# Performance work log

Measured on AMD Instinct MI355X. Metric: run time of the kernel, lower is better.

## Reference

```python
import jax, jax.numpy as jnp
import numpy as np

WINDOW = 512
STEP = 256
N_FREQ = 256
EPS = 1e-8


def setup_inputs() -> dict:
    key = jax.random.key(0)
    k1, k2, k3 = jax.random.split(key, 3)
    audio = jax.random.normal(k1, (512, 32768), dtype=jnp.float32)
    basis_real = jax.random.normal(k2, (N_FREQ, WINDOW), dtype=jnp.float32)
    basis_imag = jax.random.normal(k3, (N_FREQ, WINDOW), dtype=jnp.float32)
    return {"audio": audio, "basis_real": basis_real, "basis_imag": basis_imag}


def reference(audio, basis_real, basis_imag):
    # --- framing (windowed_audio): strided unfold -> [B, n_frames, WINDOW] ---
    n_samples = audio.shape[-1]
    n_frames = (n_samples - WINDOW) // STEP + 1  # 127 for 32768 samples
    idx = jnp.arange(n_frames)[:, None] * STEP + jnp.arange(WINDOW)[None, :]
    windowed = audio[:, idx]  # [B, F, W]

    # --- per-frame L2 normalization ---
    norms = jnp.linalg.norm(windowed, axis=-1, keepdims=True)  # [B, F, 1]
    wn = windowed / (norms + EPS)

    # --- basis normalization by complex L2 norm over window dim ---
    bnorm = jnp.sqrt(jnp.sum(basis_real * basis_real + basis_imag * basis_imag,
                             axis=-1, keepdims=True))  # [K, 1]
    br = basis_real / (bnorm + EPS)
    bi = basis_imag / (bnorm + EPS)

    # --- projection: windowed @ basis.T, real and imag parts ---
    real = jnp.einsum('bfw,kw->bfk', wn, br)  # [B, F, K]
    imag = jnp.einsum('bfw,kw->bfk', wn, bi)  # [B, F, K]
    return norms, real, imag
```

## Files before the change

### kernel.cpp

```cpp
#include <hip/hip_runtime.h>

#define WINDOW   512
#define STEPSZ   256
#define NFRAMES  127
#define NSAMP    32768
#define NBATCH   512
#define NFREQ    256
#define BM       64
#define SAMP_TILE 16640

typedef __attribute__((ext_vector_type(8))) short short8;
typedef __attribute__((ext_vector_type(4))) short bf16x4;
typedef __attribute__((ext_vector_type(4))) float f32x4;
typedef __attribute__((ext_vector_type(4))) float f4;

static __device__ __forceinline__ short f2bf(float x) {
    union { float f; unsigned u; } v; v.f = x;
    unsigned r = (v.u + 0x7fffu + ((v.u >> 16) & 1u)) >> 16;
    return (short)r;
}
static __device__ __forceinline__ float bf2f(short h) {
    union { unsigned u; float f; } v; v.u = ((unsigned)(unsigned short)h) << 16;
    return v.f;
}

__global__ __launch_bounds__(256) void prep_kernel(const float* __restrict__ br,
                                                   const float* __restrict__ bi,
                                                   short* __restrict__ Bf) {
    const int lane = threadIdx.x & 63;
    const int wid  = threadIdx.x >> 6;
    const int k    = blockIdx.x * 4 + wid;
    const float* pr = br + (size_t)k * WINDOW + lane * 8;
    const float* pi = bi + (size_t)k * WINDOW + lane * 8;
    f4 r0 = *(const f4*)pr;
    f4 r1 = *(const f4*)(pr + 4);
    f4 i0 = *(const f4*)pi;
    f4 i1 = *(const f4*)(pi + 4);
    float ss = 0.f;
#pragma unroll
    for (int j = 0; j < 4; ++j)
        ss += r0[j]*r0[j] + r1[j]*r1[j] + i0[j]*i0[j] + i1[j]*i1[j];
#pragma unroll
    for (int d = 1; d < 64; d <<= 1) ss += __shfl_xor(ss, d, 64);
    const float inv = 1.0f / (sqrtf(ss) + 1e-8f);
    short8 hr, hi;
#pragma unroll
    for (int j = 0; j < 4; ++j) {
        hr[j]     = f2bf(r0[j] * inv);
        hr[j + 4] = f2bf(r1[j] * inv);
        hi[j]     = f2bf(i0[j] * inv);
        hi[j + 4] = f2bf(i1[j] * inv);
    }
    const int kk = lane >> 2, kgrp = lane & 3;
    const int rl  = k & 15;
    const int ntR = k >> 4;
    const int ntI = 16 + (k >> 4);
    *(short8*)(Bf + ((size_t)(ntR * 16 + kk) * 64 + kgrp * 16 + rl) * 8) = hr;
    *(short8*)(Bf + ((size_t)(ntI * 16 + kk) * 64 + kgrp * 16 + rl) * 8) = hi;
}

__global__ __launch_bounds__(1024, 4) void mel_kernel(const float* __restrict__ audio,
                                                      const short* __restrict__ Bf,
                                                      float* __restrict__ out) {
    __shared__ short smp[SAMP_TILE];
    __shared__ float invn[BM];

    const int tid  = threadIdx.x;
    const int lane = tid & 63;
    const int wid  = tid >> 6;

    const int b   = blockIdx.x >> 1;
    const int mt0 = blockIdx.x & 1;
    const int f0  = mt0 * BM;

    float* out_norms = out;
    float* out_real  = out + 65024;
    float* out_imag  = out + 65024 + 16646144;

    const float* abase = audio + (size_t)b * NSAMP + f0 * STEPSZ;
    const int smax = NSAMP - f0 * STEPSZ - 4;

#pragma unroll
    for (int it = 0; it < 5; ++it) {
        const int sl = it * 4096 + tid * 4;
        if (sl < SAMP_TILE) {
            const int slc = sl < smax ? sl : smax;
            f4 v = *(const f4*)(abase + slc);
            bf16x4 h;
#pragma unroll
            for (int q = 0; q < 4; ++q) h[q] = f2bf(v[q]);
            const int byt = sl * 2;
            const int swz = byt ^ (((byt >> 9) & 7) << 4);
            *(bf16x4*)((char*)smp + swz) = h;
        }
    }
    __syncthreads();

    {
        const int f = tid >> 4, q = tid & 15;
        float ss = 0.f;
#pragma unroll
        for (int j = 0; j < 4; ++j) {
            const int byt = (f * 256 + q * 32 + j * 8) * 2;
            const int swz = byt ^ (((byt >> 9) & 7) << 4);
            short8 hv = *(const short8*)((const char*)smp + swz);
#pragma unroll
            for (int e = 0; e < 8; ++e) { const float x = bf2f(hv[e]); ss += x * x; }
        }
        ss += __shfl_xor(ss, 1, 64);
        ss += __shfl_xor(ss, 2, 64);
        ss += __shfl_xor(ss, 4, 64);
        ss += __shfl_xor(ss, 8, 64);
        const float nrm = sqrtf(ss);
        if (q == 0) {
            const int fr = f0 + f;
            if (fr < NFRAMES) out_norms[b * NFRAMES + fr] = nrm;
            invn[f] = 1.0f / (nrm + 1e-8f);
        }
    }
    __syncthreads();

    const int rlane = lane & 15;
    const int kgrp  = lane >> 4;
    const int ntg0  = wid * 2;

    f32x4 acc[4][2];
#pragma unroll
    for (int mt = 0; mt < 4; ++mt) { acc[mt][0] = (f32x4)0.f; acc[mt][1] = (f32x4)0.f; }

    const short* bp0 = Bf + ((size_t)(ntg0 + 0) * 16 * 64 + lane) * 8;
    const short* bp1 = Bf + ((size_t)(ntg0 + 1) * 16 * 64 + lane) * 8;
    short8 b0 = *(const short8*)bp0;
    short8 b1 = *(const short8*)bp1;

#pragma unroll 4
    for (int kk = 0; kk < 16; ++kk) {
        short8 a0, a1, a2, a3;
        {
            const int kb = kk * 64 + kgrp * 16;
            int byt;
            byt = (0 * 16 + rlane) * 512 + kb; a0 = *(const short8*)((const char*)smp + (byt ^ (((byt >> 9) & 7) << 4)));
            byt = (1 * 16 + rlane) * 512 + kb; a1 = *(const short8*)((const char*)smp + (byt ^ (((byt >> 9) & 7) << 4)));
            byt = (2 * 16 + rlane) * 512 + kb; a2 = *(const short8*)((const char*)smp + (byt ^ (((byt >> 9) & 7) << 4)));
            byt = (3 * 16 + rlane) * 512 + kb; a3 = *(const short8*)((const char*)smp + (byt ^ (((byt >> 9) & 7) << 4)));
        }
        short8 nb0 = b0, nb1 = b1;
        if (kk < 15) {
            nb0 = *(const short8*)(bp0 + (size_t)(kk + 1) * 512);
            nb1 = *(const short8*)(bp1 + (size_t)(kk + 1) * 512);
        }
        acc[0][0] = __builtin_amdgcn_mfma_f32_16x16x32_bf16(a0, b0, acc[0][0], 0, 0, 0);
        acc[1][0] = __builtin_amdgcn_mfma_f32_16x16x32_bf16(a1, b0, acc[1][0], 0, 0, 0);
        acc[2][0] = __builtin_amdgcn_mfma_f32_16x16x32_bf16(a2, b0, acc[2][0], 0, 0, 0);
        acc[3][0] = __builtin_amdgcn_mfma_f32_16x16x32_bf16(a3, b0, acc[3][0], 0, 0, 0);
        acc[0][1] = __builtin_amdgcn_mfma_f32_16x16x32_bf16(a0, b1, acc[0][1], 0, 0, 0);
        acc[1][1] = __builtin_amdgcn_mfma_f32_16x16x32_bf16(a1, b1, acc[1][1], 0, 0, 0);
        acc[2][1] = __builtin_amdgcn_mfma_f32_16x16x32_bf16(a2, b1, acc[2][1], 0, 0, 0);
        acc[3][1] = __builtin_amdgcn_mfma_f32_16x16x32_bf16(a3, b1, acc[3][1], 0, 0, 0);
        b0 = nb0; b1 = nb1;
    }

#pragma unroll
    for (int mt = 0; mt < 4; ++mt) {
        const int rbase = mt * 16 + kgrp * 4;
#pragma unroll
        for (int nt = 0; nt < 2; ++nt) {
            const int n = (ntg0 + nt) * 16 + rlane;
            float* dst = (n < NFREQ) ? out_real : out_imag;
            const int kcol = n & (NFREQ - 1);
#pragma unroll
            for (int j = 0; j < 4; ++j) {
                const int r  = rbase + j;
                const int fr = f0 + r;
                if (fr < NFRAMES)
                    dst[((size_t)b * NFRAMES + fr) * NFREQ + kcol] = acc[mt][nt][j] * invn[r];
            }
        }
    }
}

extern "C" void kernel_launch(void* const* d_in, const int* in_sizes, int n_in,
                              void* d_out, int out_size, void* d_ws, size_t ws_size,
                              hipStream_t stream) {
    const float* audio = (const float*)d_in[0];
    const float* br    = (const float*)d_in[1];
    const float* bi    = (const float*)d_in[2];
    float* out = (float*)d_out;
    short* Bf  = (short*)d_ws;

    prep_kernel<<<64, 256, 0, stream>>>(br, bi, Bf);
    mel_kernel<<<NBATCH * 2, 1024, 0, stream>>>(audio, Bf, out);
}
```

Measured before the change: 68.48 us.

## Fuse frame norm computation into audio staging and simplify swizzled LDS addressing

The audio staging loop now loads 8 floats per thread and accumulates squared sums in fp32 while converting to bf16. Per-256-sample partial sums go to shared memory, and frame norms are formed by adding two adjacent chunks. This removes the separate LDS re-read pass and one barrier. The basis prefetch is hoisted before staging, the MMA loop is fully unrolled with precomputed swizzle XORs, and a barrier is added before the epilogue so invn is visible. The norm is now computed from fp32 values rather than bf16-rounded ones, which changes numerics slightly.

```diff
diff --git a/kernel.cpp b/kernel.cpp
--- a/kernel.cpp
+++ b/kernel.cpp
@@ -8,9 +8,9 @@
 #define NFREQ    256
 #define BM       64
 #define SAMP_TILE 16640
+#define NPS      65
 
 typedef __attribute__((ext_vector_type(8))) short short8;
-typedef __attribute__((ext_vector_type(4))) short bf16x4;
 typedef __attribute__((ext_vector_type(4))) float f32x4;
 typedef __attribute__((ext_vector_type(4))) float f4;
 
@@ -18,10 +18,6 @@
     union { float f; unsigned u; } v; v.f = x;
     unsigned r = (v.u + 0x7fffu + ((v.u >> 16) & 1u)) >> 16;
     return (short)r;
-}
-static __device__ __forceinline__ float bf2f(short h) {
-    union { unsigned u; float f; } v; v.u = ((unsigned)(unsigned short)h) << 16;
-    return v.f;
 }
 
 __global__ __launch_bounds__(256) void prep_kernel(const float* __restrict__ br,
@@ -63,6 +59,7 @@
                                                       const short* __restrict__ Bf,
                                                       float* __restrict__ out) {
     __shared__ short smp[SAMP_TILE];
+    __shared__ float ps[NPS];
     __shared__ float invn[BM];
 
     const int tid  = threadIdx.x;
@@ -78,72 +75,69 @@
     float* out_imag  = out + 65024 + 16646144;
 
     const float* abase = audio + (size_t)b * NSAMP + f0 * STEPSZ;
-    const int smax = NSAMP - f0 * STEPSZ - 4;
+    const int smax = NSAMP - f0 * STEPSZ - 8;
+
+    const int rlane = lane & 15;
+    const int kgrp  = lane >> 4;
+    const int ntg0  = wid * 2;
+    const short* bp0 = Bf + ((size_t)(ntg0 + 0) * 16 * 64 + lane) * 8;
+    const short* bp1 = Bf + ((size_t)(ntg0 + 1) * 16 * 64 + lane) * 8;
+    short8 b0 = *(const short8*)bp0;
+    short8 b1 = *(const short8*)bp1;
 
 #pragma unroll
-    for (int it = 0; it < 5; ++it) {
-        const int sl = it * 4096 + tid * 4;
+    for (int it = 0; it < 3; ++it) {
+        const int sl = it * 8192 + tid * 8;
+        float ss = 0.f;
         if (sl < SAMP_TILE) {
             const int slc = sl < smax ? sl : smax;
-            f4 v = *(const f4*)(abase + slc);
-            bf16x4 h;
+            f4 v0 = *(const f4*)(abase + slc);
+            f4 v1 = *(const f4*)(abase + slc + 4);
+            short8 h;
 #pragma unroll
-            for (int q = 0; q < 4; ++q) h[q] = f2bf(v[q]);
+            for (int q = 0; q < 4; ++q) {
+                ss += v0[q]*v0[q] + v1[q]*v1[q];
+                h[q]     = f2bf(v0[q]);
+                h[q + 4] = f2bf(v1[q]);
+            }
             const int byt = sl * 2;
             const int swz = byt ^ (((byt >> 9) & 7) << 4);
-            *(bf16x4*)((char*)smp + swz) = h;
-        }
-    }
-    __syncthreads();
-
-    {
-        const int f = tid >> 4, q = tid & 15;
-        float ss = 0.f;
-#pragma unroll
-        for (int j = 0; j < 4; ++j) {
-            const int byt = (f * 256 + q * 32 + j * 8) * 2;
-            const int swz = byt ^ (((byt >> 9) & 7) << 4);
-            short8 hv = *(const short8*)((const char*)smp + swz);
-#pragma unroll
-            for (int e = 0; e < 8; ++e) { const float x = bf2f(hv[e]); ss += x * x; }
+            *(short8*)((char*)smp + swz) = h;
         }
         ss += __shfl_xor(ss, 1, 64);
         ss += __shfl_xor(ss, 2, 64);
         ss += __shfl_xor(ss, 4, 64);
         ss += __shfl_xor(ss, 8, 64);
-        const float nrm = sqrtf(ss);
-        if (q == 0) {
-            const int fr = f0 + f;
-            if (fr < NFRAMES) out_norms[b * NFRAMES + fr] = nrm;
-            invn[f] = 1.0f / (nrm + 1e-8f);
-        }
+        ss += __shfl_xor(ss, 16, 64);
+        const int chunk = (it * 8192 + tid * 8) >> 8;
+        if ((tid & 31) == 0 && chunk < NPS) ps[chunk] = ss;
     }
     __syncthreads();
 
-    const int rlane = lane & 15;
-    const int kgrp  = lane >> 4;
-    const int ntg0  = wid * 2;
+    if (tid < BM) {
+        const float nrm = sqrtf(ps[tid] + ps[tid + 1]);
+        const int fr = f0 + tid;
+        if (fr < NFRAMES) out_norms[b * NFRAMES + fr] = nrm;
+        invn[tid] = 1.0f / (nrm + 1e-8f);
+    }
+
+    const int rb = rlane * 512 + kgrp * 16;
+    const int X0 = (rlane & 7) << 4;
+    const int X1 = ((rlane + 1) & 7) << 4;
+    const char* sb = (const char*)smp;
 
     f32x4 acc[4][2];
 #pragma unroll
     for (int mt = 0; mt < 4; ++mt) { acc[mt][0] = (f32x4)0.f; acc[mt][1] = (f32x4)0.f; }
 
-    const short* bp0 = Bf + ((size_t)(ntg0 + 0) * 16 * 64 + lane) * 8;
-    const short* bp1 = Bf + ((size_t)(ntg0 + 1) * 16 * 64 + lane) * 8;
-    short8 b0 = *(const short8*)bp0;
-    short8 b1 = *(const short8*)bp1;
-
-#pragma unroll 4
+#pragma unroll
     for (int kk = 0; kk < 16; ++kk) {
-        short8 a0, a1, a2, a3;
-        {
-            const int kb = kk * 64 + kgrp * 16;
-            int byt;
-            byt = (0 * 16 + rlane) * 512 + kb; a0 = *(const short8*)((const char*)smp + (byt ^ (((byt >> 9) & 7) << 4)));
-            byt = (1 * 16 + rlane) * 512 + kb; a1 = *(const short8*)((const char*)smp + (byt ^ (((byt >> 9) & 7) << 4)));
-            byt = (2 * 16 + rlane) * 512 + kb; a2 = *(const short8*)((const char*)smp + (byt ^ (((byt >> 9) & 7) << 4)));
-            byt = (3 * 16 + rlane) * 512 + kb; a3 = *(const short8*)((const char*)smp + (byt ^ (((byt >> 9) & 7) << 4)));
-        }
+        const int X  = (kk < 8) ? X0 : X1;
+        const int kb = kk * 64;
+        short8 a0 = *(const short8*)(sb + (((rb + 0 * 8192) + kb) ^ X));
+        short8 a1 = *(const short8*)(sb + (((rb + 1 * 8192) + kb) ^ X));
+        short8 a2 = *(const short8*)(sb + (((rb + 2 * 8192) + kb) ^ X));
+        short8 a3 = *(const short8*)(sb + (((rb + 3 * 8192) + kb) ^ X));
         short8 nb0 = b0, nb1 = b1;
         if (kk < 15) {
             nb0 = *(const short8*)(bp0 + (size_t)(kk + 1) * 512);
@@ -159,6 +153,7 @@
         acc[3][1] = __builtin_amdgcn_mfma_f32_16x16x32_bf16(a3, b1, acc[3][1], 0, 0, 0);
         b0 = nb0; b1 = nb1;
     }
+    __syncthreads();
 
 #pragma unroll
     for (int mt = 0; mt < 4; ++mt) {
```

Result: no change. 67.68 us (-1.2%).
